# Optimization experiments

Hardware: AMD Instinct MI355X
Metric: run time of the kernel (lower is better)

Reference implementation:

```python
import jax, jax.numpy as jnp
import numpy as np

B, SQ, D = 4, 2048, 1536
HEADS, KV_HEADS, HEAD_DIM = 24, 12, 64
CROSS_DIM = 768
TEXT_LEN, NUM_TOKENS = 512, 64
ENC_LEN = TEXT_LEN + NUM_TOKENS
ROT_DIM = 32
IP_SCALE = 1.0
SCALE = 1.0 / np.sqrt(HEAD_DIM).astype(np.float32)


def _split_heads(x, n_heads):
    # [B, S, n_heads*HEAD_DIM] -> [B, n_heads, S, HEAD_DIM]
    b, s, _ = x.shape
    return x.reshape(b, s, n_heads, HEAD_DIM).transpose(0, 2, 1, 3)


def _repeat_kv(x):
    # [B, KV_HEADS, S, D] -> [B, HEADS, S, D] (repeat_interleave on head dim)
    return jnp.repeat(x, HEADS // KV_HEADS, axis=1)


def _apply_rope(x, cos, sin):
    # x: [B, H, S, ROT_DIM]; cos/sin: [S, ROT_DIM]; use_real_unbind_dim=-2 convention
    xr = x.reshape(*x.shape[:-1], 2, ROT_DIM // 2)
    x_real, x_imag = xr[..., 0, :], xr[..., 1, :]
    x_rot = jnp.concatenate([-x_imag, x_real], axis=-1)
    return x * cos[None, None] + x_rot * sin[None, None]


def _attn(q, k, v):
    scores = jnp.einsum('bhqd,bhkd->bhqk', q, k) * SCALE
    probs = jax.nn.softmax(scores.astype(jnp.float32), axis=-1).astype(q.dtype)
    return jnp.einsum('bhqk,bhkd->bhqd', probs, v)


def setup_inputs():
    key = jax.random.key(0)
    ks = jax.random.split(key, 10)
    t = jnp.arange(SQ, dtype=jnp.float32)
    freqs = 1.0 / (10000.0 ** (jnp.arange(ROT_DIM // 2, dtype=jnp.float32) / (ROT_DIM // 2)))
    ang = t[:, None] * freqs[None, :]  # [SQ, ROT_DIM//2]
    rope_cos = jnp.concatenate([jnp.cos(ang), jnp.cos(ang)], axis=-1)
    rope_sin = jnp.concatenate([jnp.sin(ang), jnp.sin(ang)], axis=-1)
    s = 0.02
    return {
        'hidden_states': jax.random.normal(ks[0], (B, SQ, D), jnp.float32),
        'encoder_hidden_states': jax.random.normal(ks[1], (B, ENC_LEN, CROSS_DIM), jnp.float32),
        'rope_cos': rope_cos,
        'rope_sin': rope_sin,
        'wq': jax.random.normal(ks[2], (D, HEADS * HEAD_DIM), jnp.float32) * s,
        'wk': jax.random.normal(ks[3], (CROSS_DIM, KV_HEADS * HEAD_DIM), jnp.float32) * s,
        'wv': jax.random.normal(ks[4], (CROSS_DIM, KV_HEADS * HEAD_DIM), jnp.float32) * s,
        'wk_ip': jax.random.normal(ks[5], (CROSS_DIM, KV_HEADS * HEAD_DIM), jnp.float32) * s,
        'wv_ip': jax.random.normal(ks[6], (CROSS_DIM, KV_HEADS * HEAD_DIM), jnp.float32) * s,
        'wo': jax.random.normal(ks[7], (HEADS * HEAD_DIM, D), jnp.float32) * s,
        'bo': jnp.zeros((D,), jnp.float32),
    }


def reference(hidden_states, encoder_hidden_states, rope_cos, rope_sin,
              wq, wk, wv, wk_ip, wv_ip, wo, bo):
    residual = hidden_states
    text = encoder_hidden_states[:, :TEXT_LEN, :]
    ip = encoder_hidden_states[:, TEXT_LEN:, :]

    q = _split_heads(hidden_states @ wq, HEADS)          # [B, H, SQ, Dh]
    k = _repeat_kv(_split_heads(text @ wk, KV_HEADS))    # [B, H, St, Dh]
    v = _repeat_kv(_split_heads(text @ wv, KV_HEADS))

    # RoPE in float32 on first ROT_DIM channels of Q only (cross-attention)
    q32 = q.astype(jnp.float32)
    q_rot = _apply_rope(q32[..., :ROT_DIM], rope_cos, rope_sin)
    q = jnp.concatenate([q_rot, q32[..., ROT_DIM:]], axis=-1).astype(hidden_states.dtype)

    out = _attn(q, k, v)                                 # [B, H, SQ, Dh]

    # IP-adapter branch
    ip_k = _repeat_kv(_split_heads(ip @ wk_ip, KV_HEADS))  # [B, H, NUM_TOKENS, Dh]
    ip_v = _repeat_kv(_split_heads(ip @ wv_ip, KV_HEADS))
    out = out + IP_SCALE * _attn(q, ip_k, ip_v)

    out = out.transpose(0, 2, 1, 3).reshape(B, SQ, HEADS * HEAD_DIM)
    out = out @ wo + bo
    return out + residual
```

## Files before the change

### kernel.cpp

```cpp
#include <hip/hip_runtime.h>
#include <hip/hip_bf16.h>

typedef __attribute__((ext_vector_type(8))) short short8;
typedef __attribute__((ext_vector_type(4))) short short4v;
typedef __attribute__((ext_vector_type(4))) float f32x4;

#define MFMA16(a, b, c) __builtin_amdgcn_mfma_f32_16x16x32_bf16(a, b, c, 0, 0, 0)
#define QK_SCALE_LOG2E 0.18033688011112042f

__device__ __forceinline__ short f2bf(float x) {
  union { float f; unsigned u; } v; v.f = x;
  unsigned u = v.u;
  u += 0x7FFFu + ((u >> 16) & 1u);
  return (short)(u >> 16);
}
__device__ __forceinline__ short f2bf_trunc(float x) {
  union { float f; unsigned u; } v; v.f = x;
  return (short)(v.u >> 16);
}

__device__ __forceinline__ void gload16(const void* g, void* l) {
  __builtin_amdgcn_global_load_lds(
      (const __attribute__((address_space(1))) unsigned int*)g,
      (__attribute__((address_space(3))) unsigned int*)l, 16, 0, 0);
}

__global__ __launch_bounds__(256) void enc_pack_kernel(
    const float* __restrict__ enc, short* __restrict__ text,
    short* __restrict__ ip) {
  int i4 = blockIdx.x * 256 + threadIdx.x;
  int i = i4 * 4;
  if (i >= 4 * 576 * 768) return;
  int c = i % 768;
  int rs = i / 768;
  int b = rs / 576, s = rs % 576;
  f32x4 v = *(const f32x4*)(enc + i);
  short4v o;
  o[0] = f2bf(v[0]); o[1] = f2bf(v[1]); o[2] = f2bf(v[2]); o[3] = f2bf(v[3]);
  if (s < 512)
    *(short4v*)(text + (size_t)(b * 512 + s) * 768 + c) = o;
  else
    *(short4v*)(ip + (size_t)(b * 64 + (s - 512)) * 768 + c) = o;
}

__global__ __launch_bounds__(256) void prep_weights_kernel(
    const float* __restrict__ wq, const float* __restrict__ wo,
    const float* __restrict__ wk, const float* __restrict__ wv,
    const float* __restrict__ wkip, const float* __restrict__ wvip,
    short* __restrict__ wqT, short* __restrict__ woT,
    short* __restrict__ wkvT, short* __restrict__ wkvipT) {
  __shared__ float tile[32][33];
  const int z = blockIdx.z;
  const float* src; short* dst; int N, row_off;
  if (z == 0)      { src = wq;   dst = wqT;    N = 1536; row_off = 0; }
  else if (z == 1) { src = wo;   dst = woT;    N = 1536; row_off = 0; }
  else if (z == 2) { src = wk;   dst = wkvT;   N = 768;  row_off = 0; }
  else if (z == 3) { src = wv;   dst = wkvT;   N = 768;  row_off = 768; }
  else if (z == 4) { src = wkip; dst = wkvipT; N = 768;  row_off = 0; }
  else             { src = wvip; dst = wkvipT; N = 768;  row_off = 768; }
  int c0 = blockIdx.x * 32, r0 = blockIdx.y * 32;
  if (c0 >= N || r0 >= N) return;
  int tx = threadIdx.x & 31, ty = threadIdx.x >> 5;
#pragma unroll
  for (int j = 0; j < 4; ++j)
    tile[ty + j * 8][tx] = src[(size_t)(r0 + ty + j * 8) * N + c0 + tx];
  __syncthreads();
#pragma unroll
  for (int j = 0; j < 4; ++j)
    dst[(size_t)(row_off + c0 + ty + j * 8) * N + r0 + tx] =
        f2bf(tile[tx][ty + j * 8]);
}

__device__ __forceinline__ void stage32(const short* __restrict__ gA,
                                        const short* __restrict__ gBt,
                                        int lda, int ldb, char* buf, int tid) {
#pragma unroll
  for (int li = 0; li < 2; ++li) {
    int L = li * 4096 + tid * 16;
    int row = L >> 6;
    int cb = (L & 63) ^ (((row >> 1) & 3) << 4);
    gload16(gA + (size_t)row * lda + (cb >> 1), buf + L);
    gload16(gBt + (size_t)row * ldb + (cb >> 1), buf + 8192 + L);
  }
}

__device__ __forceinline__ void compute32(const char* p0, int wr, int wc,
                                          int lr, int hk, int xr,
                                          f32x4 acc[4][4]) {
  short8 af[4], bf[4];
#pragma unroll
  for (int m = 0; m < 4; ++m) {
    int row = wr + m * 16 + lr;
    af[m] = *(const short8*)(p0 + row * 64 + (hk ^ xr));
  }
#pragma unroll
  for (int n = 0; n < 4; ++n) {
    int row = wc + n * 16 + lr;
    bf[n] = *(const short8*)(p0 + 8192 + row * 64 + (hk ^ xr));
  }
#pragma unroll
  for (int m = 0; m < 4; ++m)
#pragma unroll
    for (int n = 0; n < 4; ++n) acc[m][n] = MFMA16(af[m], bf[n], acc[m][n]);
}

template <int K>
__device__ __forceinline__ void gemm128p(
    const short* __restrict__ A, const short* __restrict__ Bt, int lda,
    int ldb, int row0, int col0, char* sm, f32x4 acc[4][4]) {
  const int tid = threadIdx.x;
  const int lane = tid & 63, wid = tid >> 6;
  const int wr = (wid >> 1) * 64, wc = (wid & 1) * 64;
  const int lr = lane & 15;
  const int hk = (lane >> 4) * 16;
  const int xr = ((lr >> 1) & 3) << 4;
  constexpr int NT = K / 32;

  const short* gA = A + (size_t)row0 * lda;
  const short* gB = Bt + (size_t)col0 * ldb;

  char* p0 = sm;
  char* p1 = sm + 16384;
  char* p2 = sm + 32768;

  stage32(gA, gB, lda, ldb, p0, tid);
  stage32(gA + 32, gB + 32, lda, ldb, p1, tid);
  asm volatile("s_waitcnt vmcnt(4)" ::: "memory");
  __builtin_amdgcn_s_barrier();

  for (int t = 0; t < NT; ++t) {
    if (t + 2 < NT)
      stage32(gA + (t + 2) * 32, gB + (t + 2) * 32, lda, ldb, p2, tid);
    __builtin_amdgcn_sched_barrier(0);
    compute32(p0, wr, wc, lr, hk, xr, acc);
    __builtin_amdgcn_sched_barrier(0);
    if (t + 2 < NT)
      asm volatile("s_waitcnt vmcnt(4)" ::: "memory");
    else
      asm volatile("s_waitcnt vmcnt(0)" ::: "memory");
    __builtin_amdgcn_s_barrier();
    char* tmp = p0; p0 = p1; p1 = p2; p2 = tmp;
  }
}

__device__ __forceinline__ void grid128(int& row0, int& col0) {
  int bid = blockIdx.x;
  int x = bid & 7;
  int j = bid >> 3;
  row0 = (x * 8 + (j & 7)) * 128;
  col0 = (j >> 3) * 128;
}

__device__ __forceinline__ void q_issueA(const float* __restrict__ gAf,
                                         int tid, f32x4 ar[4]) {
#pragma unroll
  for (int li = 0; li < 2; ++li) {
    int L = li * 4096 + tid * 16;
    int row = L >> 6;
    int cb = (L & 63) ^ (((row >> 1) & 3) << 4);
    const float* src = gAf + (size_t)row * 1536 + (cb >> 1);
    ar[li * 2] = *(const f32x4*)src;
    ar[li * 2 + 1] = *(const f32x4*)(src + 4);
  }
}
__device__ __forceinline__ void q_writeA(char* buf, int tid, const f32x4 ar[4]) {
#pragma unroll
  for (int li = 0; li < 2; ++li) {
    int L = li * 4096 + tid * 16;
    short8 s;
#pragma unroll
    for (int j = 0; j < 4; ++j) {
      s[j] = f2bf_trunc(ar[li * 2][j]);
      s[j + 4] = f2bf_trunc(ar[li * 2 + 1][j]);
    }
    *(short8*)(buf + L) = s;
  }
}
__device__ __forceinline__ void q_stageB(const short* __restrict__ gBt,
                                         char* buf, int tid) {
#pragma unroll
  for (int li = 0; li < 2; ++li) {
    int L = li * 4096 + tid * 16;
    int row = L >> 6;
    int cb = (L & 63) ^ (((row >> 1) & 3) << 4);
    gload16(gBt + (size_t)row * 1536 + (cb >> 1), buf + 8192 + L);
  }
}

__global__ __launch_bounds__(256, 3) void q_proj_128p(
    const float* __restrict__ hs, const short* __restrict__ wqT,
    const float* __restrict__ rc, const float* __restrict__ rsn,
    short* __restrict__ qbuf) {
  __shared__ char sm[49152];
  f32x4 acc[4][4] = {};
  int row0, col0;
  grid128(row0, col0);

  const int tid = threadIdx.x;
  const int lane = tid & 63, wid = tid >> 6;
  const int wr = (wid >> 1) * 64, wc = (wid & 1) * 64;
  const int lr = lane & 15;
  const int hk = (lane >> 4) * 16;
  const int xr = ((lr >> 1) & 3) << 4;
  constexpr int NT = 48;

  const float* gAf = hs + (size_t)row0 * 1536;
  const short* gB = wqT + (size_t)col0 * 1536;
  char* p0 = sm;
  char* p1 = sm + 16384;
  char* p2 = sm + 32768;
  f32x4 arA[4], arB[4];

  q_issueA(gAf, tid, arA);
  q_stageB(gB, p0, tid);
  q_issueA(gAf + 32, tid, arB);
  q_stageB(gB + 32, p1, tid);
  asm volatile("s_waitcnt vmcnt(8)" ::: "memory");
  q_writeA(p0, tid, arA);
  asm volatile("s_waitcnt vmcnt(6) lgkmcnt(0)" ::: "memory");
  __builtin_amdgcn_s_barrier();

  for (int t = 0; t < NT; ++t) {
    if (t + 2 < NT) {
      if ((t & 1) == 0) q_issueA(gAf + (t + 2) * 32, tid, arA);
      else              q_issueA(gAf + (t + 2) * 32, tid, arB);
      q_stageB(gB + (t + 2) * 32, p2, tid);
    }
    __builtin_amdgcn_sched_barrier(0);
    compute32(p0, wr, wc, lr, hk, xr, acc);
    __builtin_amdgcn_sched_barrier(0);
    if (t + 2 < NT)
      asm volatile("s_waitcnt vmcnt(6)" ::: "memory");
    else
      asm volatile("s_waitcnt vmcnt(0)" ::: "memory");
    if (t + 1 < NT) {
      if ((t & 1) == 0) q_writeA(p1, tid, arB);
      else              q_writeA(p1, tid, arA);
    }
    asm volatile("s_waitcnt lgkmcnt(0)" ::: "memory");
    __builtin_amdgcn_s_barrier();
    char* tmp = p0; p0 = p1; p1 = p2; p2 = tmp;
  }

  const int lrow4 = (lane >> 4) * 4;
  const int h = (col0 + wc) >> 6;
#pragma unroll
  for (int m = 0; m < 4; ++m) {
#pragma unroll
    for (int r = 0; r < 4; ++r) {
      int grow = row0 + wr + m * 16 + lrow4 + r;
      int b = grow >> 11, t = grow & 2047;
      float v0 = acc[m][0][r], v1 = acc[m][1][r];
      float c0 = rc[t * 32 + lr], s0 = rsn[t * 32 + lr];
      float c1 = rc[t * 32 + 16 + lr], s1 = rsn[t * 32 + 16 + lr];
      float n0 = (v0 * c0 - v1 * s0) * QK_SCALE_LOG2E;
      float n1 = (v1 * c1 + v0 * s1) * QK_SCALE_LOG2E;
      short* ob = qbuf + ((size_t)(b * 24 + h) * 2048 + t) * 64;
      ob[lr] = f2bf(n0);
      ob[16 + lr] = f2bf(n1);
      ob[32 + lr] = f2bf(acc[m][2][r] * QK_SCALE_LOG2E);
      ob[48 + lr] = f2bf(acc[m][3][r] * QK_SCALE_LOG2E);
    }
  }
}

__global__ __launch_bounds__(256, 3) void o_proj_128p(
    const short* __restrict__ attnbf, const short* __restrict__ woT,
    const float* __restrict__ bo, const float* __restrict__ resid,
    float* __restrict__ out) {
  __shared__ char sm[49152];
  f32x4 acc[4][4] = {};
  int row0, col0;
  grid128(row0, col0);
  gemm128p<1536>(attnbf, woT, 1536, 1536, row0, col0, sm, acc);

  const int lane = threadIdx.x & 63, wid = threadIdx.x >> 6;
  const int wr = (wid >> 1) * 64, wc = (wid & 1) * 64;
  const int lr = lane & 15, lrow4 = (lane >> 4) * 4;
#pragma unroll
  for (int m = 0; m < 4; ++m) {
#pragma unroll
    for (int n = 0; n < 4; ++n) {
#pragma unroll
      for (int r = 0; r < 4; ++r) {
        int grow = row0 + wr + m * 16 + lrow4 + r;
        int gcol = col0 + wc + n * 16 + lr;
        size_t off = (size_t)grow * 1536 + gcol;
        out[off] = acc[m][n][r] + bo[gcol] + resid[off];
      }
    }
  }
}

__global__ __launch_bounds__(256, 3) void kv_gemm(
    const short* __restrict__ Abf, const short* __restrict__ wkvT,
    short* __restrict__ kout, short* __restrict__ vtout, int rlog2) {
  __shared__ char sm[49152];
  f32x4 acc[4][4] = {};
  const int row0 = blockIdx.y * 128, col0 = blockIdx.x * 128;
  gemm128p<768>(Abf, wkvT, 768, 768, row0, col0, sm, acc);

  const int tid = threadIdx.x;
  const int lane = tid & 63, wid = tid >> 6;
  const int wr = (wid >> 1) * 64, wc = (wid & 1) * 64;
  const int lr = lane & 15, lrow4 = (lane >> 4) * 4;
  const int rmask = (1 << rlog2) - 1;
#pragma unroll
  for (int m = 0; m < 4; ++m) {
#pragma unroll
    for (int n = 0; n < 4; ++n) {
#pragma unroll
      for (int r = 0; r < 4; ++r) {
        int grow = row0 + wr + m * 16 + lrow4 + r;
        int gcol = col0 + wc + n * 16 + lr;
        int b = grow >> rlog2, key = grow & rmask;
        short val = f2bf(acc[m][n][r]);
        if (gcol < 768) {
          int kvh = gcol >> 6, d = gcol & 63;
          kout[((((size_t)(b * 12 + kvh)) << rlog2) + key) * 64 + d] = val;
        } else {
          int c2 = gcol - 768;
          int kvh = c2 >> 6, d = c2 & 63;
          int kp = (key & ~31) | (((key >> 2) & 3) << 3) |
                   (((key >> 4) & 1) << 2) | (key & 3);
          vtout[(((size_t)((b * 12 + kvh) * 64 + d)) << rlog2) + kp] = val;
        }
      }
    }
  }
}

__device__ __forceinline__ void stage_tile(const short* __restrict__ ks,
                                           const short* __restrict__ vs,
                                           int vstr, short* kb, short* vb,
                                           int tid) {
#pragma unroll
  for (int q = 0; q < 2; ++q) {
    int L = q * 4096 + tid * 16;
    int row = L >> 7;
    int sc = ((L & 127) ^ ((row & 7) << 4)) >> 1;
    gload16(ks + row * 64 + sc, (char*)kb + L);
    gload16(vs + (size_t)row * vstr + sc, (char*)vb + L);
  }
}

__device__ __forceinline__ void attn_tile(const short* kb, const short* vb,
                                          const short8 qf[2],
                                          float& m_run, float& l_run,
                                          f32x4 o_acc[4], int lane) {
  const int lr = lane & 15, hi = lane >> 4;
  f32x4 s[4];
#pragma unroll
  for (int nf = 0; nf < 4; ++nf) {
    int row = nf * 16 + lr;
    int rx = (row & 7) << 4;
    const char* base = (const char*)kb + row * 128;
    short8 k0 = *(const short8*)(base + ((hi * 16) ^ rx));
    short8 k1 = *(const short8*)(base + ((64 + hi * 16) ^ rx));
    f32x4 a = {0.f, 0.f, 0.f, 0.f};
    a = MFMA16(k0, qf[0], a);
    a = MFMA16(k1, qf[1], a);
    s[nf] = a;
  }
  float mx = fmaxf(fmaxf(s[0][0], s[0][1]), fmaxf(s[0][2], s[0][3]));
#pragma unroll
  for (int nf = 1; nf < 4; ++nf)
    mx = fmaxf(mx, fmaxf(fmaxf(s[nf][0], s[nf][1]), fmaxf(s[nf][2], s[nf][3])));
  if (__any(mx - m_run > 8.0f)) {
    float mr = fmaxf(mx, __shfl_xor(mx, 16));
    mr = fmaxf(mr, __shfl_xor(mr, 32));
    float mn = fmaxf(m_run, mr);
    float corr = __builtin_amdgcn_exp2f(m_run - mn);
    m_run = mn;
    l_run *= corr;
#pragma unroll
    for (int r = 0; r < 4; ++r) {
      float cr = __shfl(corr, hi * 4 + r);
#pragma unroll
      for (int no = 0; no < 4; ++no) o_acc[no][r] *= cr;
    }
  }
  short8 pa[2];
#pragma unroll
  for (int nf = 0; nf < 4; ++nf) {
#pragma unroll
    for (int r = 0; r < 4; ++r) {
      float p = __builtin_amdgcn_exp2f(s[nf][r] - m_run);
      l_run += p;
      pa[nf >> 1][(nf & 1) * 4 + r] = f2bf_trunc(p);
    }
  }
#pragma unroll
  for (int ks = 0; ks < 2; ++ks) {
#pragma unroll
    for (int no = 0; no < 4; ++no) {
      int row = no * 16 + lr;
      int rx = (row & 7) << 4;
      short8 vf = *(const short8*)((const char*)vb + row * 128 +
                                   ((ks * 64 + hi * 16) ^ rx));
      o_acc[no] = MFMA16(pa[ks], vf, o_acc[no]);
    }
  }
}

__global__ __launch_bounds__(256, 4) void attn_kernel(
    const short* __restrict__ qbuf, const short* __restrict__ kbuf,
    const short* __restrict__ vtbuf, const short* __restrict__ kipbuf,
    const short* __restrict__ vtipbuf, short* __restrict__ attn_out) {
  const int tid = threadIdx.x;
  const int lane = tid & 63, wid = tid >> 6;
  const int f = (blockIdx.x & 7) * 384 + (blockIdx.x >> 3);
  const int qt = f & 31;
  const int h = (f >> 5) % 24;
  const int b = f / (32 * 24);
  const int kvh = h >> 1;
  const int lr = lane & 15, hi = lane >> 4;

  __shared__ short skv_k[2 * 64 * 64];
  __shared__ short skv_v[2 * 64 * 64];

  const short* qp = qbuf + (size_t)(b * 24 + h) * 2048 * 64;
  const short* kp = kbuf + (size_t)(b * 12 + kvh) * 512 * 64;
  const short* vp = vtbuf + (size_t)(b * 12 + kvh) * 64 * 512;
  const short* kip = kipbuf + (size_t)(b * 12 + kvh) * 64 * 64;
  const short* vip = vtipbuf + (size_t)(b * 12 + kvh) * 64 * 64;

  const int q0 = qt * 64 + wid * 16;
  short8 qf[2];
  qf[0] = *(const short8*)(qp + (size_t)(q0 + lr) * 64 + hi * 8);
  qf[1] = *(const short8*)(qp + (size_t)(q0 + lr) * 64 + 32 + hi * 8);

  float m1 = -1.0e30f, l1 = 0.f, m2 = -1.0e30f, l2 = 0.f;
  f32x4 oacc1[4] = {}, oacc2[4] = {};

  stage_tile(kp, vp, 512, skv_k, skv_v, tid);
  __syncthreads();

  for (int t = 0; t < 9; ++t) {
    int cur = t & 1, nxt = cur ^ 1;
    if (t < 8) {
      const short* ks_ = (t < 7) ? kp + (t + 1) * 64 * 64 : kip;
      const short* vs_ = (t < 7) ? vp + (t + 1) * 64 : vip;
      int vstr = (t < 7) ? 512 : 64;
      stage_tile(ks_, vs_, vstr, skv_k + nxt * 4096, skv_v + nxt * 4096, tid);
    }
    if (t < 8)
      attn_tile(skv_k + cur * 4096, skv_v + cur * 4096, qf, m1, l1, oacc1, lane);
    else
      attn_tile(skv_k + cur * 4096, skv_v + cur * 4096, qf, m2, l2, oacc2, lane);
    __syncthreads();
  }

  l1 += __shfl_xor(l1, 16); l1 += __shfl_xor(l1, 32);
  l2 += __shfl_xor(l2, 16); l2 += __shfl_xor(l2, 32);
  float inv1 = 1.0f / l1, inv2 = 1.0f / l2;
#pragma unroll
  for (int r = 0; r < 4; ++r) {
    float i1 = __shfl(inv1, hi * 4 + r);
    float i2 = __shfl(inv2, hi * 4 + r);
    int grow = b * 2048 + q0 + hi * 4 + r;
#pragma unroll
    for (int no = 0; no < 4; ++no) {
      float val = oacc1[no][r] * i1 + oacc2[no][r] * i2;
      attn_out[(size_t)grow * 1536 + h * 64 + no * 16 + lr] = f2bf(val);
    }
  }
}

extern "C" void kernel_launch(void* const* d_in, const int* in_sizes, int n_in,
                              void* d_out, int out_size, void* d_ws, size_t ws_size,
                              hipStream_t stream) {
  const float* hs = (const float*)d_in[0];
  const float* enc = (const float*)d_in[1];
  const float* rc = (const float*)d_in[2];
  const float* rsn = (const float*)d_in[3];
  const float* wq = (const float*)d_in[4];
  const float* wk = (const float*)d_in[5];
  const float* wv = (const float*)d_in[6];
  const float* wkip = (const float*)d_in[7];
  const float* wvip = (const float*)d_in[8];
  const float* wo = (const float*)d_in[9];
  const float* bo = (const float*)d_in[10];
  float* out = (float*)d_out;

  char* ws = (char*)d_ws;
  short* attnbuf = (short*)(ws + 0);
  short* qbuf    = (short*)(ws + 25165824);
  short* kbuf    = (short*)(ws + 50331648);
  short* vtbuf   = (short*)(ws + 53477376);
  short* kipbuf  = (short*)(ws + 56623104);
  short* vtipbuf = (short*)(ws + 57016320);
  short* textbf  = (short*)(ws + 57409536);
  short* ipbf    = (short*)(ws + 60555264);
  short* wqT     = (short*)(ws + 60948480);
  short* woT     = (short*)(ws + 65667072);
  short* wkvT    = (short*)(ws + 70385664);
  short* wkvipT  = (short*)(ws + 72744960);

  enc_pack_kernel<<<1728, 256, 0, stream>>>(enc, textbf, ipbf);
  prep_weights_kernel<<<dim3(48, 48, 6), 256, 0, stream>>>(
      wq, wo, wk, wv, wkip, wvip, wqT, woT, wkvT, wkvipT);

  q_proj_128p<<<768, 256, 0, stream>>>(hs, wqT, rc, rsn, qbuf);
  kv_gemm<<<dim3(12, 16), 256, 0, stream>>>(textbf, wkvT, kbuf, vtbuf, 9);
  kv_gemm<<<dim3(12, 2), 256, 0, stream>>>(ipbf, wkvipT, kipbuf, vtipbuf, 6);

  attn_kernel<<<3072, 256, 0, stream>>>(qbuf, kbuf, vtbuf, kipbuf,
                                        vtipbuf, attnbuf);

  o_proj_128p<<<768, 256, 0, stream>>>(attnbuf, woT, bo, hs, out);
}
```

Baseline: 203.4 us.

## Triple-buffer attention K/V staging and merge text/IP KV projection launches

Result: faster. 188.5 us (-7.3%).

```diff
diff --git a/kernel.cpp b/kernel.cpp
--- a/kernel.cpp
+++ b/kernel.cpp
@@ -118,7 +118,6 @@
 
   const short* gA = A + (size_t)row0 * lda;
   const short* gB = Bt + (size_t)col0 * ldb;
-
   char* p0 = sm;
   char* p1 = sm + 16384;
   char* p2 = sm + 32768;
@@ -292,13 +291,22 @@
   }
 }
 
-__global__ __launch_bounds__(256, 3) void kv_gemm(
-    const short* __restrict__ Abf, const short* __restrict__ wkvT,
-    short* __restrict__ kout, short* __restrict__ vtout, int rlog2) {
+__global__ __launch_bounds__(256, 3) void kv_gemm_all(
+    const short* __restrict__ textbf, const short* __restrict__ ipbf,
+    const short* __restrict__ wkvT, const short* __restrict__ wkvipT,
+    short* __restrict__ kbuf, short* __restrict__ vtbuf,
+    short* __restrict__ kipbuf, short* __restrict__ vtipbuf) {
   __shared__ char sm[49152];
   f32x4 acc[4][4] = {};
-  const int row0 = blockIdx.y * 128, col0 = blockIdx.x * 128;
-  gemm128p<768>(Abf, wkvT, 768, 768, row0, col0, sm, acc);
+  const bool ip = blockIdx.y >= 16;
+  const short* Abf = ip ? ipbf : textbf;
+  const short* W = ip ? wkvipT : wkvT;
+  short* kout = ip ? kipbuf : kbuf;
+  short* vtout = ip ? vtipbuf : vtbuf;
+  const int rlog2 = ip ? 6 : 9;
+  const int row0 = (ip ? (blockIdx.y - 16) : blockIdx.y) * 128;
+  const int col0 = blockIdx.x * 128;
+  gemm128p<768>(Abf, W, 768, 768, row0, col0, sm, acc);
 
   const int tid = threadIdx.x;
   const int lane = tid & 63, wid = tid >> 6;
@@ -403,7 +411,7 @@
   }
 }
 
-__global__ __launch_bounds__(256, 4) void attn_kernel(
+__global__ __launch_bounds__(256, 3) void attn_kernel(
     const short* __restrict__ qbuf, const short* __restrict__ kbuf,
     const short* __restrict__ vtbuf, const short* __restrict__ kipbuf,
     const short* __restrict__ vtipbuf, short* __restrict__ attn_out) {
@@ -416,8 +424,8 @@
   const int kvh = h >> 1;
   const int lr = lane & 15, hi = lane >> 4;
 
-  __shared__ short skv_k[2 * 64 * 64];
-  __shared__ short skv_v[2 * 64 * 64];
+  __shared__ short skv_k[3 * 64 * 64];
+  __shared__ short skv_v[3 * 64 * 64];
 
   const short* qp = qbuf + (size_t)(b * 24 + h) * 2048 * 64;
   const short* kp = kbuf + (size_t)(b * 12 + kvh) * 512 * 64;
@@ -434,21 +442,31 @@
   f32x4 oacc1[4] = {}, oacc2[4] = {};
 
   stage_tile(kp, vp, 512, skv_k, skv_v, tid);
-  __syncthreads();
+  stage_tile(kp + 64 * 64, vp + 64, 512, skv_k + 4096, skv_v + 4096, tid);
+  asm volatile("s_waitcnt vmcnt(4)" ::: "memory");
+  __builtin_amdgcn_s_barrier();
 
   for (int t = 0; t < 9; ++t) {
-    int cur = t & 1, nxt = cur ^ 1;
-    if (t < 8) {
-      const short* ks_ = (t < 7) ? kp + (t + 1) * 64 * 64 : kip;
-      const short* vs_ = (t < 7) ? vp + (t + 1) * 64 : vip;
-      int vstr = (t < 7) ? 512 : 64;
-      stage_tile(ks_, vs_, vstr, skv_k + nxt * 4096, skv_v + nxt * 4096, tid);
-    }
+    if (t + 2 <= 8) {
+      int tt = t + 2;
+      const short* ks_ = (tt < 8) ? kp + tt * 64 * 64 : kip;
+      const short* vs_ = (tt < 8) ? vp + tt * 64 : vip;
+      int vstr = (tt < 8) ? 512 : 64;
+      int bsel = tt % 3;
+      stage_tile(ks_, vs_, vstr, skv_k + bsel * 4096, skv_v + bsel * 4096, tid);
+    }
+    __builtin_amdgcn_sched_barrier(0);
+    int cur = t % 3;
     if (t < 8)
       attn_tile(skv_k + cur * 4096, skv_v + cur * 4096, qf, m1, l1, oacc1, lane);
     else
       attn_tile(skv_k + cur * 4096, skv_v + cur * 4096, qf, m2, l2, oacc2, lane);
-    __syncthreads();
+    __builtin_amdgcn_sched_barrier(0);
+    if (t + 2 <= 8)
+      asm volatile("s_waitcnt vmcnt(4)" ::: "memory");
+    else if (t + 1 <= 8)
+      asm volatile("s_waitcnt vmcnt(0)" ::: "memory");
+    __builtin_amdgcn_s_barrier();
   }
 
   l1 += __shfl_xor(l1, 16); l1 += __shfl_xor(l1, 32);
@@ -502,8 +520,8 @@
       wq, wo, wk, wv, wkip, wvip, wqT, woT, wkvT, wkvipT);
 
   q_proj_128p<<<768, 256, 0, stream>>>(hs, wqT, rc, rsn, qbuf);
-  kv_gemm<<<dim3(12, 16), 256, 0, stream>>>(textbf, wkvT, kbuf, vtbuf, 9);
-  kv_gemm<<<dim3(12, 2), 256, 0, stream>>>(ipbf, wkvipT, kipbuf, vtipbuf, 6);
+  kv_gemm_all<<<dim3(12, 18), 256, 0, stream>>>(textbf, ipbf, wkvT, wkvipT,
+                                                kbuf, vtbuf, kipbuf, vtipbuf);
 
   attn_kernel<<<3072, 256, 0, stream>>>(qbuf, kbuf, vtbuf, kipbuf,
                                         vtipbuf, attnbuf);
```
